# Optimization experiments

Hardware: AMD Instinct MI355X
Metric: run time of the kernel (lower is better)

## Reference

```python
import jax, jax.numpy as jnp
import numpy as np

T = 8192
D_IN = 64          # state_dim + action_dim = 48 + 16
H = 2048           # hidden_size
OUT = 49           # state_dim + 1


def _glorot(key, shape):
    # eqx.nn.Linear default init: uniform(-1/sqrt(in), 1/sqrt(in))
    lim = 1.0 / np.sqrt(shape[-1])
    return jax.random.uniform(key, shape, jnp.float32, -lim, lim)


def setup_inputs() -> dict:
    key = jax.random.key(0)
    ks = jax.random.split(key, 14)
    x = jax.random.normal(ks[0], (T, D_IN), jnp.float32)
    enc_w = _glorot(ks[1], (H, D_IN))
    enc_b = _glorot(ks[2], (H,))
    # GRUCell params (eqx layout: [3H, in]/[3H, H], gate order: reset, update, new)
    w_ih = _glorot(ks[3], (3 * H, H))
    w_hh = _glorot(ks[4], (3 * H, H))
    b_ih = _glorot(ks[5], (3 * H,))
    b_n = _glorot(ks[6], (H,))
    # MLP decoder: depth=2, width=H, relu activations, identity final
    mlp_w0 = _glorot(ks[7], (H, H))
    mlp_b0 = _glorot(ks[8], (H,))
    mlp_w1 = _glorot(ks[9], (H, H))
    mlp_b1 = _glorot(ks[10], (H,))
    mlp_w2 = _glorot(ks[11], (OUT, H))
    mlp_b2 = _glorot(ks[12], (OUT,))
    return {"x": x, "enc_w": enc_w, "enc_b": enc_b, "w_ih": w_ih, "w_hh": w_hh,
            "b_ih": b_ih, "b_n": b_n, "mlp_w0": mlp_w0, "mlp_b0": mlp_b0,
            "mlp_w1": mlp_w1, "mlp_b1": mlp_b1, "mlp_w2": mlp_w2, "mlp_b2": mlp_b2}


def reference(x, enc_w, enc_b, w_ih, w_hh, b_ih, b_n,
              mlp_w0, mlp_b0, mlp_w1, mlp_b1, mlp_w2, mlp_b2):
    # encode: vmapped Linear over time -> [T, H]
    xe = x @ enc_w.T + enc_b
    # input-side gate pre-activations for all steps (hoisted out of the scan)
    igates = (xe @ w_ih.T + b_ih).reshape(T, 3, H)  # [T, 3, H]

    def cell(h, ig):
        hg = (w_hh @ h).reshape(3, H)
        r = jax.nn.sigmoid(ig[0] + hg[0])            # reset gate
        z = jax.nn.sigmoid(ig[1] + hg[1])            # update gate
        n = jnp.tanh(ig[2] + r * (hg[2] + b_n))      # candidate
        h_new = n + z * (h - n)                      # eqx GRUCell update
        return h_new, h_new

    h0 = jnp.zeros((H,), x.dtype)
    _, hs = jax.lax.scan(cell, h0, igates)           # hs: [T, H]

    # decode: MLP(H -> OUT, width H, depth 2, relu)
    h = jax.nn.relu(hs @ mlp_w0.T + mlp_b0)
    h = jax.nn.relu(h @ mlp_w1.T + mlp_b1)
    outs = h @ mlp_w2.T + mlp_b2                     # [T, OUT]
    return outs
```

## Files before the change

kernel.cpp:

```cpp
#include <hip/hip_runtime.h>
#include <math.h>

#define T_STEPS 8192
#define HID 2048
#define H3 6144
#define NBLK 256
#define CHUNK 2048

typedef float f32x4 __attribute__((ext_vector_type(4)));

__device__ __forceinline__ float4 cload_f4(const float* p) {
    float4 r;
    asm volatile("global_load_dwordx4 %0, %1, off sc0 sc1\n\t"
                 "s_waitcnt vmcnt(0)"
                 : "=&v"(r) : "v"(p) : "memory");
    return r;
}
__device__ __forceinline__ void cstore_f4(float4* p, float x, float y,
                                          float z, float w) {
    f32x4 v; v[0] = x; v[1] = y; v[2] = z; v[3] = w;
    asm volatile("global_store_dwordx4 %0, %1, off sc0 sc1"
                 :: "v"(p), "v"(v) : "memory");
}

template<int RELU>
__global__ __launch_bounds__(256) void sgemm_bias(
    const float* __restrict__ A, const float* __restrict__ B,
    const float* __restrict__ bias, float* __restrict__ C,
    int M, int N, int K)
{
    __shared__ float As[16][64];
    __shared__ float Bs[16][64];
    const int tid = threadIdx.x;
    const int tm = tid & 15;
    const int tn = tid >> 4;
    const int m0 = blockIdx.y * 64;
    const int n0 = blockIdx.x * 64;
    const int lm = tid >> 2;
    const int lk = (tid & 3) * 4;

    float c[4][4] = {};

    for (int k0 = 0; k0 < K; k0 += 16) {
        float4 av = *(const float4*)(A + (size_t)(m0 + lm) * K + k0 + lk);
        float4 bv = make_float4(0.f, 0.f, 0.f, 0.f);
        const int bn = n0 + lm;
        if (bn < N) bv = *(const float4*)(B + (size_t)bn * K + k0 + lk);
        __syncthreads();
        As[lk+0][lm] = av.x; As[lk+1][lm] = av.y; As[lk+2][lm] = av.z; As[lk+3][lm] = av.w;
        Bs[lk+0][lm] = bv.x; Bs[lk+1][lm] = bv.y; Bs[lk+2][lm] = bv.z; Bs[lk+3][lm] = bv.w;
        __syncthreads();
        #pragma unroll
        for (int kk = 0; kk < 16; kk++) {
            float4 a4 = *(const float4*)&As[kk][tm * 4];
            float4 b4 = *(const float4*)&Bs[kk][tn * 4];
            c[0][0] += a4.x * b4.x; c[0][1] += a4.x * b4.y; c[0][2] += a4.x * b4.z; c[0][3] += a4.x * b4.w;
            c[1][0] += a4.y * b4.x; c[1][1] += a4.y * b4.y; c[1][2] += a4.y * b4.z; c[1][3] += a4.y * b4.w;
            c[2][0] += a4.z * b4.x; c[2][1] += a4.z * b4.y; c[2][2] += a4.z * b4.z; c[2][3] += a4.z * b4.w;
            c[3][0] += a4.w * b4.x; c[3][1] += a4.w * b4.y; c[3][2] += a4.w * b4.z; c[3][3] += a4.w * b4.w;
        }
    }

    const int mrow = m0 + tm * 4;
    #pragma unroll
    for (int i = 0; i < 4; i++) {
        #pragma unroll
        for (int j = 0; j < 4; j++) {
            const int n = n0 + tn * 4 + j;
            if (n < N) {
                float v = c[i][j] + bias[n];
                if (RELU) v = fmaxf(v, 0.f);
                C[(size_t)(mrow + i) * N + n] = v;
            }
        }
    }
}

__global__ __launch_bounds__(256) void sgemm_nn(
    const float* __restrict__ A, const float* __restrict__ B,
    float* __restrict__ C, int M, int N, int K)
{
    __shared__ float As[16][64];
    __shared__ float Bs[16][64];
    const int tid = threadIdx.x;
    const int tm = tid & 15;
    const int tn = tid >> 4;
    const int m0 = blockIdx.y * 64;
    const int n0 = blockIdx.x * 64;
    const int lm = tid >> 2;
    const int lk = (tid & 3) * 4;
    const int bk  = tid >> 4;
    const int bn4 = (tid & 15) * 4;

    float c[4][4] = {};

    for (int k0 = 0; k0 < K; k0 += 16) {
        float4 av = *(const float4*)(A + (size_t)(m0 + lm) * K + k0 + lk);
        float4 bv = *(const float4*)(B + (size_t)(k0 + bk) * N + n0 + bn4);
        __syncthreads();
        As[lk+0][lm] = av.x; As[lk+1][lm] = av.y; As[lk+2][lm] = av.z; As[lk+3][lm] = av.w;
        *(float4*)&Bs[bk][bn4] = bv;
        __syncthreads();
        #pragma unroll
        for (int kk = 0; kk < 16; kk++) {
            float4 a4 = *(const float4*)&As[kk][tm * 4];
            float4 b4 = *(const float4*)&Bs[kk][tn * 4];
            c[0][0] += a4.x * b4.x; c[0][1] += a4.x * b4.y; c[0][2] += a4.x * b4.z; c[0][3] += a4.x * b4.w;
            c[1][0] += a4.y * b4.x; c[1][1] += a4.y * b4.y; c[1][2] += a4.y * b4.z; c[1][3] += a4.y * b4.w;
            c[2][0] += a4.z * b4.x; c[2][1] += a4.z * b4.y; c[2][2] += a4.z * b4.z; c[2][3] += a4.z * b4.w;
            c[3][0] += a4.w * b4.x; c[3][1] += a4.w * b4.y; c[3][2] += a4.w * b4.z; c[3][3] += a4.w * b4.w;
        }
    }

    const int mrow = m0 + tm * 4;
    #pragma unroll
    for (int i = 0; i < 4; i++) {
        #pragma unroll
        for (int j = 0; j < 4; j++)
            C[(size_t)(mrow + i) * N + n0 + tn * 4 + j] = c[i][j];
    }
}

__global__ __launch_bounds__(256) void bcomb_kernel(
    const float* __restrict__ w_ih, const float* __restrict__ enc_b,
    const float* __restrict__ b_ih, float* __restrict__ b_comb)
{
    const int wv = threadIdx.x >> 6, lane = threadIdx.x & 63;
    const int r = blockIdx.x * 4 + wv;
    const float* row = w_ih + (size_t)r * HID;
    float acc = 0.f;
    for (int j = lane; j < HID; j += 64) acc += row[j] * enc_b[j];
    #pragma unroll
    for (int m = 32; m >= 1; m >>= 1) acc += __shfl_xor(acc, m, 64);
    if (lane == 0) b_comb[r] = acc + b_ih[r];
}

__global__ __launch_bounds__(1024, 4) void gru_scan(
    const float* __restrict__ w_hh, const float* __restrict__ b_n,
    const float* __restrict__ ig,
    float* __restrict__ hs,
    float4* __restrict__ atoms,
    int base, int steps)
{
    __shared__ float h_lds[HID];
    __shared__ float pg[16][3];
    __shared__ float hg_lds[24];
    const int tid  = threadIdx.x;
    const int lane = tid & 63;
    const int w    = tid >> 6;
    const int pr   = tid & 127;
    const int k    = tid >> 7;
    const int b    = blockIdx.x;

    float4 wreg[3][4];
    #pragma unroll
    for (int j = 0; j < 3; j++) {
        const int idx3 = 3 * k + j;
        const float* wp = w_hh +
            (size_t)((idx3 >> 3) * HID + b * 8 + (idx3 & 7)) * HID;
        #pragma unroll
        for (int m = 0; m < 4; m++)
            wreg[j][m] = *(const float4*)(wp + 4 * pr + 512 * m);
    }

    const int i = b * 8 + tid;
    const float bn = (tid < 8) ? b_n[i] : 0.f;

    for (int t = 0; t < steps; t++) {
        float ig0 = 0.f, ig1 = 0.f, ig2 = 0.f;
        if (tid < 8) {
            const float* p = ig + (size_t)t * H3 + i;
            ig0 = p[0]; ig1 = p[HID]; ig2 = p[2 * HID];
        }

        const float target = (float)(base + t);
        const float* ap = (const float*)(atoms + (t & 1) * 1024 + tid);
        float4 f;
        do { f = cload_f4(ap); } while (f.z < target);
        *(float2*)&h_lds[2 * tid] = make_float2(f.x, f.y);
        __syncthreads();

        float a0 = 0.f, a1 = 0.f, a2 = 0.f;
        #pragma unroll
        for (int m = 0; m < 4; m++) {
            float4 h4 = *(const float4*)&h_lds[4 * pr + 512 * m];
            a0 += wreg[0][m].x * h4.x + wreg[0][m].y * h4.y + wreg[0][m].z * h4.z + wreg[0][m].w * h4.w;
            a1 += wreg[1][m].x * h4.x + wreg[1][m].y * h4.y + wreg[1][m].z * h4.z + wreg[1][m].w * h4.w;
            a2 += wreg[2][m].x * h4.x + wreg[2][m].y * h4.y + wreg[2][m].z * h4.z + wreg[2][m].w * h4.w;
        }
        #pragma unroll
        for (int s = 32; s >= 1; s >>= 1) {
            a0 += __shfl_xor(a0, s, 64);
            a1 += __shfl_xor(a1, s, 64);
            a2 += __shfl_xor(a2, s, 64);
        }
        if (lane == 0) { pg[w][0] = a0; pg[w][1] = a1; pg[w][2] = a2; }
        __syncthreads();

        if (w == 0) {
            if (lane < 24) {
                const int kk = lane / 3, j = lane - 3 * kk;
                hg_lds[lane] = pg[2 * kk][j] + pg[2 * kk + 1][j];
            }
            asm volatile("s_waitcnt lgkmcnt(0)" ::: "memory");
            float h_new = 0.f;
            if (lane < 8) {
                const float r = 1.f / (1.f + expf(-(ig0 + hg_lds[lane])));
                const float z = 1.f / (1.f + expf(-(ig1 + hg_lds[8 + lane])));
                const float n = tanhf(ig2 + r * (hg_lds[16 + lane] + bn));
                const float hp = h_lds[i];
                h_new = n + z * (hp - n);
                hs[(size_t)t * HID + i] = h_new;
            }
            const float ha = __shfl(h_new, lane * 2, 64);
            const float hb = __shfl(h_new, lane * 2 + 1, 64);
            if (lane < 4) {
                cstore_f4(atoms + ((t + 1) & 1) * 1024 + b * 4 + lane,
                          ha, hb, (float)(base + t + 1), 0.f);
            }
        }
    }
}

extern "C" void kernel_launch(void* const* d_in, const int* in_sizes, int n_in,
                              void* d_out, int out_size, void* d_ws, size_t ws_size,
                              hipStream_t stream) {
    const float* x     = (const float*)d_in[0];
    const float* enc_w = (const float*)d_in[1];
    const float* enc_b = (const float*)d_in[2];
    const float* w_ih  = (const float*)d_in[3];
    const float* w_hh  = (const float*)d_in[4];
    const float* b_ih  = (const float*)d_in[5];
    const float* b_n   = (const float*)d_in[6];
    const float* w0    = (const float*)d_in[7];
    const float* b0    = (const float*)d_in[8];
    const float* w1    = (const float*)d_in[9];
    const float* b1    = (const float*)d_in[10];
    const float* w2    = (const float*)d_in[11];
    const float* b2    = (const float*)d_in[12];
    float* out = (float*)d_out;

    float* R1    = (float*)d_ws;
    float* R2    = R1 + (size_t)16777216;
    float* wcomb = R2 + (size_t)16777216;
    float* bcomb = wcomb + 393216;
    float4* atoms = (float4*)(bcomb + 6144);

    (void)hipMemsetAsync(atoms, 0, 2 * 1024 * sizeof(float4), stream);

    sgemm_nn<<<dim3(1, 96), 256, 0, stream>>>(w_ih, enc_w, wcomb, 6144, 64, 2048);
    bcomb_kernel<<<dim3(1536), 256, 0, stream>>>(w_ih, enc_b, b_ih, bcomb);

    for (int c = 0; c < T_STEPS / CHUNK; c++) {
        sgemm_bias<0><<<dim3(H3 / 64, CHUNK / 64), 256, 0, stream>>>(
            x + (size_t)c * CHUNK * 64, wcomb, bcomb, R1, CHUNK, H3, 64);
        gru_scan<<<dim3(NBLK), dim3(1024), 0, stream>>>(
            w_hh, b_n, R1, R2 + (size_t)c * CHUNK * HID, atoms, c * CHUNK, CHUNK);
    }

    sgemm_bias<1><<<dim3(HID / 64, T_STEPS / 64), 256, 0, stream>>>(
        R2, w0, b0, R1, T_STEPS, HID, HID);
    sgemm_bias<1><<<dim3(HID / 64, T_STEPS / 64), 256, 0, stream>>>(
        R1, w1, b1, R2, T_STEPS, HID, HID);
    sgemm_bias<0><<<dim3(1, T_STEPS / 64), 256, 0, stream>>>(
        R2, w2, b2, out, T_STEPS, 49, 2048);
}
```

Measured before the change: 27.31 ms.

## Distribute GRU gate math across wave pairs and use per-element flag atoms

```diff
diff --git a/kernel.cpp b/kernel.cpp
--- a/kernel.cpp
+++ b/kernel.cpp
@@ -8,6 +8,7 @@
 #define CHUNK 2048
 
 typedef float f32x4 __attribute__((ext_vector_type(4)));
+typedef float f32x2 __attribute__((ext_vector_type(2)));
 
 __device__ __forceinline__ float4 cload_f4(const float* p) {
     float4 r;
@@ -16,10 +17,9 @@
                  : "=&v"(r) : "v"(p) : "memory");
     return r;
 }
-__device__ __forceinline__ void cstore_f4(float4* p, float x, float y,
-                                          float z, float w) {
-    f32x4 v; v[0] = x; v[1] = y; v[2] = z; v[3] = w;
-    asm volatile("global_store_dwordx4 %0, %1, off sc0 sc1"
+__device__ __forceinline__ void cstore_f2(float2* p, float x, float y) {
+    f32x2 v; v[0] = x; v[1] = y;
+    asm volatile("global_store_dwordx2 %0, %1, off sc0 sc1"
                  :: "v"(p), "v"(v) : "memory");
 }
 
@@ -139,12 +139,11 @@
     const float* __restrict__ w_hh, const float* __restrict__ b_n,
     const float* __restrict__ ig,
     float* __restrict__ hs,
-    float4* __restrict__ atoms,
+    float2* __restrict__ atoms,
     int base, int steps)
 {
     __shared__ float h_lds[HID];
     __shared__ float pg[16][3];
-    __shared__ float hg_lds[24];
     const int tid  = threadIdx.x;
     const int lane = tid & 63;
     const int w    = tid >> 6;
@@ -154,30 +153,29 @@
 
     float4 wreg[3][4];
     #pragma unroll
-    for (int j = 0; j < 3; j++) {
-        const int idx3 = 3 * k + j;
-        const float* wp = w_hh +
-            (size_t)((idx3 >> 3) * HID + b * 8 + (idx3 & 7)) * HID;
+    for (int g = 0; g < 3; g++) {
+        const float* wp = w_hh + (size_t)(g * HID + b * 8 + k) * HID;
         #pragma unroll
         for (int m = 0; m < 4; m++)
-            wreg[j][m] = *(const float4*)(wp + 4 * pr + 512 * m);
-    }
-
-    const int i = b * 8 + tid;
-    const float bn = (tid < 8) ? b_n[i] : 0.f;
+            wreg[g][m] = *(const float4*)(wp + 4 * pr + 512 * m);
+    }
+
+    const int  i       = b * 8 + k;
+    const bool gate_th = ((tid & 127) == 0);
+    const float bn = b_n[i];
 
     for (int t = 0; t < steps; t++) {
         float ig0 = 0.f, ig1 = 0.f, ig2 = 0.f;
-        if (tid < 8) {
+        if (gate_th) {
             const float* p = ig + (size_t)t * H3 + i;
             ig0 = p[0]; ig1 = p[HID]; ig2 = p[2 * HID];
         }
 
         const float target = (float)(base + t);
-        const float* ap = (const float*)(atoms + (t & 1) * 1024 + tid);
+        const float* ap = (const float*)(atoms + (size_t)(t & 1) * 2048 + 2 * tid);
         float4 f;
-        do { f = cload_f4(ap); } while (f.z < target);
-        *(float2*)&h_lds[2 * tid] = make_float2(f.x, f.y);
+        do { f = cload_f4(ap); } while (f.y < target || f.w < target);
+        *(float2*)&h_lds[2 * tid] = make_float2(f.x, f.z);
         __syncthreads();
 
         float a0 = 0.f, a1 = 0.f, a2 = 0.f;
@@ -194,31 +192,23 @@
             a1 += __shfl_xor(a1, s, 64);
             a2 += __shfl_xor(a2, s, 64);
         }
-        if (lane == 0) { pg[w][0] = a0; pg[w][1] = a1; pg[w][2] = a2; }
-        __syncthreads();
-
-        if (w == 0) {
-            if (lane < 24) {
-                const int kk = lane / 3, j = lane - 3 * kk;
-                hg_lds[lane] = pg[2 * kk][j] + pg[2 * kk + 1][j];
-            }
-            asm volatile("s_waitcnt lgkmcnt(0)" ::: "memory");
-            float h_new = 0.f;
-            if (lane < 8) {
-                const float r = 1.f / (1.f + expf(-(ig0 + hg_lds[lane])));
-                const float z = 1.f / (1.f + expf(-(ig1 + hg_lds[8 + lane])));
-                const float n = tanhf(ig2 + r * (hg_lds[16 + lane] + bn));
-                const float hp = h_lds[i];
-                h_new = n + z * (hp - n);
-                hs[(size_t)t * HID + i] = h_new;
-            }
-            const float ha = __shfl(h_new, lane * 2, 64);
-            const float hb = __shfl(h_new, lane * 2 + 1, 64);
-            if (lane < 4) {
-                cstore_f4(atoms + ((t + 1) & 1) * 1024 + b * 4 + lane,
-                          ha, hb, (float)(base + t + 1), 0.f);
-            }
-        }
+        if ((w & 1) && lane == 0) { pg[w][0] = a0; pg[w][1] = a1; pg[w][2] = a2; }
+        __syncthreads();
+
+        if (gate_th) {
+            const float hg0 = a0 + pg[w + 1][0];
+            const float hg1 = a1 + pg[w + 1][1];
+            const float hg2 = a2 + pg[w + 1][2];
+            const float r = 1.f / (1.f + expf(-(ig0 + hg0)));
+            const float z = 1.f / (1.f + expf(-(ig1 + hg1)));
+            const float n = tanhf(ig2 + r * (hg2 + bn));
+            const float hp = h_lds[i];
+            const float h_new = n + z * (hp - n);
+            hs[(size_t)t * HID + i] = h_new;
+            cstore_f2(atoms + (size_t)((t + 1) & 1) * 2048 + i,
+                      h_new, (float)(base + t + 1));
+        }
+        asm volatile("s_barrier" ::: "memory");
     }
 }
 
@@ -244,9 +234,9 @@
     float* R2    = R1 + (size_t)16777216;
     float* wcomb = R2 + (size_t)16777216;
     float* bcomb = wcomb + 393216;
-    float4* atoms = (float4*)(bcomb + 6144);
-
-    (void)hipMemsetAsync(atoms, 0, 2 * 1024 * sizeof(float4), stream);
+    float2* atoms = (float2*)(bcomb + 6144);
+
+    (void)hipMemsetAsync(atoms, 0, 2 * 2048 * sizeof(float2), stream);
 
     sgemm_nn<<<dim3(1, 96), 256, 0, stream>>>(w_ih, enc_w, wcomb, 6144, 64, 2048);
     bcomb_kernel<<<dim3(1536), 256, 0, stream>>>(w_ih, enc_b, b_ih, bcomb);
```

New measurement: 41.96 ms. 53.7% more time.

## Split GRU step sync into per-block flags plus separate hidden-state buffer

Applied to the files above, without the earlier changes.

```diff
diff --git a/kernel.cpp b/kernel.cpp
--- a/kernel.cpp
+++ b/kernel.cpp
@@ -8,19 +8,40 @@
 #define CHUNK 2048
 
 typedef float f32x4 __attribute__((ext_vector_type(4)));
-
-__device__ __forceinline__ float4 cload_f4(const float* p) {
-    float4 r;
-    asm volatile("global_load_dwordx4 %0, %1, off sc0 sc1\n\t"
+typedef float f32x2 __attribute__((ext_vector_type(2)));
+
+__device__ __forceinline__ float cload_f1(const float* p) {
+    float r;
+    asm volatile("global_load_dword %0, %1, off sc0 sc1\n\t"
                  "s_waitcnt vmcnt(0)"
                  : "=&v"(r) : "v"(p) : "memory");
     return r;
 }
-__device__ __forceinline__ void cstore_f4(float4* p, float x, float y,
-                                          float z, float w) {
-    f32x4 v; v[0] = x; v[1] = y; v[2] = z; v[3] = w;
-    asm volatile("global_store_dwordx4 %0, %1, off sc0 sc1"
-                 :: "v"(p), "v"(v) : "memory");
+__device__ __forceinline__ float2 cload_f2(const float* p) {
+    float2 r;
+    asm volatile("global_load_dwordx2 %0, %1, off sc0 sc1\n\t"
+                 "s_waitcnt vmcnt(0)"
+                 : "=&v"(r) : "v"(p) : "memory");
+    return r;
+}
+__device__ __forceinline__ void cstore_f1(float* p, float x) {
+    asm volatile("global_store_dword %0, %1, off sc0 sc1"
+                 :: "v"(p), "v"(x) : "memory");
+}
+
+#if __has_builtin(__builtin_amdgcn_exp2f)
+__device__ __forceinline__ float fexp2(float x) { return __builtin_amdgcn_exp2f(x); }
+#else
+__device__ __forceinline__ float fexp2(float x) {
+    float r; asm("v_exp_f32 %0, %1" : "=v"(r) : "v"(x)); return r;
+}
+#endif
+__device__ __forceinline__ float frcp(float x) { return __builtin_amdgcn_rcpf(x); }
+__device__ __forceinline__ float fsigmoid(float x) {
+    return frcp(1.f + fexp2(-1.44269504089f * x));
+}
+__device__ __forceinline__ float ftanh_(float x) {
+    return 2.f * frcp(1.f + fexp2(-2.88539008178f * x)) - 1.f;
 }
 
 template<int RELU>
@@ -139,7 +160,8 @@
     const float* __restrict__ w_hh, const float* __restrict__ b_n,
     const float* __restrict__ ig,
     float* __restrict__ hs,
-    float4* __restrict__ atoms,
+    float* __restrict__ h_pub,
+    float* __restrict__ flags,
     int base, int steps)
 {
     __shared__ float h_lds[HID];
@@ -174,10 +196,12 @@
         }
 
         const float target = (float)(base + t);
-        const float* ap = (const float*)(atoms + (t & 1) * 1024 + tid);
-        float4 f;
-        do { f = cload_f4(ap); } while (f.z < target);
-        *(float2*)&h_lds[2 * tid] = make_float2(f.x, f.y);
+        const int ph = t & 1;
+        const float* fp = flags + ph * 256 + (tid >> 2);
+        float f;
+        do { f = cload_f1(fp); } while (f < target);
+        float2 hv = cload_f2(h_pub + ph * 2048 + 2 * tid);
+        *(float2*)&h_lds[2 * tid] = hv;
         __syncthreads();
 
         float a0 = 0.f, a1 = 0.f, a2 = 0.f;
@@ -205,19 +229,18 @@
             asm volatile("s_waitcnt lgkmcnt(0)" ::: "memory");
             float h_new = 0.f;
             if (lane < 8) {
-                const float r = 1.f / (1.f + expf(-(ig0 + hg_lds[lane])));
-                const float z = 1.f / (1.f + expf(-(ig1 + hg_lds[8 + lane])));
-                const float n = tanhf(ig2 + r * (hg_lds[16 + lane] + bn));
+                const float r = fsigmoid(ig0 + hg_lds[lane]);
+                const float z = fsigmoid(ig1 + hg_lds[8 + lane]);
+                const float n = ftanh_(ig2 + r * (hg_lds[16 + lane] + bn));
                 const float hp = h_lds[i];
                 h_new = n + z * (hp - n);
+                cstore_f1(h_pub + ((t + 1) & 1) * 2048 + i, h_new);
+            }
+            asm volatile("s_waitcnt vmcnt(0)" ::: "memory");
+            if (lane == 0)
+                cstore_f1(flags + ((t + 1) & 1) * 256 + b, target + 1.f);
+            if (lane < 8)
                 hs[(size_t)t * HID + i] = h_new;
-            }
-            const float ha = __shfl(h_new, lane * 2, 64);
-            const float hb = __shfl(h_new, lane * 2 + 1, 64);
-            if (lane < 4) {
-                cstore_f4(atoms + ((t + 1) & 1) * 1024 + b * 4 + lane,
-                          ha, hb, (float)(base + t + 1), 0.f);
-            }
         }
     }
 }
@@ -244,9 +267,10 @@
     float* R2    = R1 + (size_t)16777216;
     float* wcomb = R2 + (size_t)16777216;
     float* bcomb = wcomb + 393216;
-    float4* atoms = (float4*)(bcomb + 6144);
-
-    (void)hipMemsetAsync(atoms, 0, 2 * 1024 * sizeof(float4), stream);
+    float* h_pub = bcomb + 6144;
+    float* flags = h_pub + 2 * 2048;
+
+    (void)hipMemsetAsync(h_pub, 0, (2 * 2048 + 2 * 256) * sizeof(float), stream);
 
     sgemm_nn<<<dim3(1, 96), 256, 0, stream>>>(w_ih, enc_w, wcomb, 6144, 64, 2048);
     bcomb_kernel<<<dim3(1536), 256, 0, stream>>>(w_ih, enc_b, b_ih, bcomb);
@@ -255,7 +279,8 @@
         sgemm_bias<0><<<dim3(H3 / 64, CHUNK / 64), 256, 0, stream>>>(
             x + (size_t)c * CHUNK * 64, wcomb, bcomb, R1, CHUNK, H3, 64);
         gru_scan<<<dim3(NBLK), dim3(1024), 0, stream>>>(
-            w_hh, b_n, R1, R2 + (size_t)c * CHUNK * HID, atoms, c * CHUNK, CHUNK);
+            w_hh, b_n, R1, R2 + (size_t)c * CHUNK * HID, h_pub, flags,
+            c * CHUNK, CHUNK);
     }
 
     sgemm_bias<1><<<dim3(HID / 64, T_STEPS / 64), 256, 0, stream>>>(
```

New measurement: 55.99 ms. 2.05x slower.
